# Kernel optimization log

Hardware: AMD Instinct MI355X
Metric: run time of the kernel (lower is better)

Reference implementation:

```python
import jax, jax.numpy as jnp
import numpy as np

B, L, F = 512, 128, 300          # batch, cycles per sample, curve length
D_MODEL = 512
D_LLM = 4096
E = 8                            # num_experts
G = 2                            # num_general_experts
TOP_K = 2
P = TOP_K / E                    # top-p threshold = topK / num_experts
EPS = 1e-9


def setup_inputs() -> dict:
    key = jax.random.key(0)
    ks = jax.random.split(key, 8)
    s_in = 1.0 / np.sqrt(3 * F).astype(np.float32)   # torch Linear init bound
    s_g = 1.0 / np.sqrt(D_LLM).astype(np.float32)
    return {
        "cycle_curve_data": jax.random.normal(ks[0], (B, L, 3, F), jnp.float32),
        "DKP_embeddings": jax.random.normal(ks[1], (B, D_LLM), jnp.float32),
        "W_exp": jax.random.uniform(ks[2], (E, 3 * F, D_MODEL), jnp.float32, -s_in, s_in),
        "b_exp": jax.random.uniform(ks[3], (E, D_MODEL), jnp.float32, -s_in, s_in),
        "W_gen": jax.random.uniform(ks[4], (G, 3 * F, D_MODEL), jnp.float32, -s_in, s_in),
        "b_gen": jax.random.uniform(ks[5], (G, D_MODEL), jnp.float32, -s_in, s_in),
        "W_gate": jax.random.uniform(ks[6], (D_LLM, E), jnp.float32, -s_g, s_g),
        "b_gate": jax.random.uniform(ks[7], (E,), jnp.float32, -s_g, s_g),
    }


def top_p_mask(logits, p):
    # softmax -> sort desc -> cumsum < p (first always kept) -> scatter back
    probs = jax.nn.softmax(logits, axis=-1)
    order = jnp.argsort(-probs, axis=-1)
    cum = jnp.cumsum(jnp.take_along_axis(probs, order, axis=-1), axis=-1)
    m = (cum < p).at[:, 0].set(True)
    rows = jnp.arange(logits.shape[0])[:, None]
    return jnp.zeros(logits.shape, bool).at[rows, order].set(m)


def reference(cycle_curve_data, DKP_embeddings, W_exp, b_exp, W_gen, b_gen, W_gate, b_gate):
    Bsz, Ls = cycle_curve_data.shape[:2]
    x = cycle_curve_data.reshape(Bsz, Ls, -1)            # [B, L, 3F]  (Flatten(start_dim=2))

    # gate (eval path: no noisy gating)
    logits = DKP_embeddings @ W_gate + b_gate            # [B, E]
    mask = top_p_mask(logits, P)
    w = jax.nn.softmax(logits, axis=1) * mask            # masked gate probs
    w = w / (jnp.sum(w, axis=1, keepdims=True) + EPS)    # renormalize (zeros stay zero)

    # dense equivalent of per-expert gather -> Linear -> weighted scatter-combine:
    # tokens with w[b,e]==0 contribute nothing, matching the sparse dispatcher.
    expert_outs = jnp.einsum('blf,efd->ebld', x, W_exp) + b_exp[:, None, None, :]  # [E,B,L,D]
    combined = jnp.einsum('be,ebld->bld', w, expert_outs).astype(jnp.bfloat16)     # [B,L,D] bf16

    # general experts run over the full batch and accumulate (bf16 + f32 -> f32)
    gen = jnp.einsum('blf,gfd->bld', x, W_gen) + jnp.sum(b_gen, axis=0)            # [B,L,D]
    return combined + gen
```

## Files before the change

kernel.cpp:

```cpp
#include <hip/hip_runtime.h>
#include <stdint.h>

#define NB   512
#define NL   128
#define NK   900
#define NKP  928
#define NKT  29
#define ND   512
#define NDLLM 4096
#define NE   8
#define ASTR 40

typedef __bf16 bf16x8 __attribute__((ext_vector_type(8)));
typedef float  f32x4  __attribute__((ext_vector_type(4)));

__device__ __forceinline__ unsigned short f2bf(float f) {
  union { float f; uint32_t u; } v; v.f = f;
  uint32_t u = v.u;
  return (unsigned short)((u + 0x7fffu + ((u >> 16) & 1u)) >> 16);
}

__global__ __launch_bounds__(256) void gate_kernel(
    const float* __restrict__ dkp,
    const float* __restrict__ Wg,
    const float* __restrict__ bg,
    int* __restrict__ eidx)
{
  const int b = blockIdx.x;
  const int t = threadIdx.x;
  float acc[8];
#pragma unroll
  for (int e = 0; e < 8; ++e) acc[e] = 0.f;
  const float* drow = dkp + (size_t)b * NDLLM;
  for (int k = t; k < NDLLM; k += 256) {
    float d = drow[k];
    const float4* w4 = (const float4*)(Wg + (size_t)k * 8);
    float4 w0 = w4[0], w1 = w4[1];
    acc[0] += d * w0.x; acc[1] += d * w0.y; acc[2] += d * w0.z; acc[3] += d * w0.w;
    acc[4] += d * w1.x; acc[5] += d * w1.y; acc[6] += d * w1.z; acc[7] += d * w1.w;
  }
#pragma unroll
  for (int e = 0; e < 8; ++e)
    for (int off = 32; off >= 1; off >>= 1)
      acc[e] += __shfl_down(acc[e], off, 64);

  __shared__ float red[4][8];
  const int wave = t >> 6, lane = t & 63;
  if (lane == 0) {
#pragma unroll
    for (int e = 0; e < 8; ++e) red[wave][e] = acc[e];
  }
  __syncthreads();
  if (t == 0) {
    float best = -1e30f; int bi = 0;
#pragma unroll
    for (int e = 0; e < 8; ++e) {
      float v = red[0][e] + red[1][e] + red[2][e] + red[3][e] + bg[e];
      if (v > best) { best = v; bi = e; }
    }
    eidx[b] = bi;
  }
}

__global__ __launch_bounds__(256) void pack_kernel(
    const float* __restrict__ Wexp,
    const float* __restrict__ Wgen,
    unsigned short* __restrict__ Wt)
{
  const int nt = blockIdx.x;
  const int kt = blockIdx.y;
  const int e  = blockIdx.z;
  const int k0 = kt * 32, n0 = nt * 64;
  __shared__ float tile[32][65];
  const int t = threadIdx.x;
#pragma unroll
  for (int i = 0; i < 8; ++i) {
    int idx = t + i * 256;
    int k = idx >> 6, n = idx & 63;
    int kg = k0 + k;
    float v = 0.f;
    if (kg < NK) {
      size_t off = (size_t)kg * ND + n0 + n;
      v = Wexp[(size_t)e * NK * ND + off] + Wgen[off] + Wgen[(size_t)NK * ND + off];
    }
    tile[k][n] = v;
  }
  __syncthreads();
#pragma unroll
  for (int i = 0; i < 8; ++i) {
    int idx = t + i * 256;
    int n = idx >> 5, k = idx & 31;
    Wt[((size_t)e * ND + n0 + n) * NKP + k0 + k] = f2bf(tile[k][n]);
  }
}

__global__ __launch_bounds__(256) void bias_kernel(
    const float* __restrict__ bexp, const float* __restrict__ bgen,
    float* __restrict__ btot)
{
  int i = blockIdx.x * 256 + threadIdx.x;
  int d = i & (ND - 1);
  btot[i] = bexp[i] + bgen[d] + bgen[ND + d];
}

__global__ __launch_bounds__(512, 2) void gemm_kernel(
    const float* __restrict__ x,
    const unsigned short* __restrict__ Wt,
    const float* __restrict__ btot,
    const int* __restrict__ eidx,
    float* __restrict__ out)
{
  __shared__ unsigned short As[2][NL * ASTR];
  __shared__ unsigned short Bs[2][ND * ASTR];

  const int b    = blockIdx.x;
  const int t    = threadIdx.x;
  const int lane = t & 63;
  const int w    = t >> 6;
  const int wm   = (w >> 2) * 64;
  const int wn   = (w & 3) * 128;
  const int ln   = lane & 15;
  const int kq   = lane >> 4;

  const int e = eidx[b];
  const float* xb = x + (size_t)b * NL * NK;
  const unsigned short* wtb = Wt + (size_t)e * ND * NKP;

  const int arow  = t >> 3;
  const int acol  = t & 7;
  const int brow  = t >> 2;
  const int bslot = t & 3;

  f32x4 acc[4][8];
  const f32x4 zero = {0.f, 0.f, 0.f, 0.f};
#pragma unroll
  for (int mi = 0; mi < 4; ++mi)
#pragma unroll
    for (int ni = 0; ni < 8; ++ni) acc[mi][ni] = zero;

  f32x4 aIn[2];
  uint4 bIn[4];

#define ISSUE_LOADS(K0)                                                       \
  {                                                                           \
    const int kg_ = (K0) + acol * 4;                                          \
    if (kg_ < NK) {                                                           \
      aIn[0] = *(const f32x4*)(xb + (size_t)arow * NK + kg_);                 \
      aIn[1] = *(const f32x4*)(xb + (size_t)(arow + 64) * NK + kg_);          \
    } else {                                                                  \
      aIn[0] = zero; aIn[1] = zero;                                           \
    }                                                                         \
    const unsigned short* bsrc_ = wtb + (K0) + bslot * 8;                     \
    _Pragma("unroll")                                                         \
    for (int p = 0; p < 4; ++p)                                               \
      bIn[p] = *(const uint4*)(bsrc_ + (size_t)(brow + p * 128) * NKP);       \
  }

#define WRITE_STAGE(BUF)                                                      \
  {                                                                           \
    _Pragma("unroll")                                                         \
    for (int p = 0; p < 2; ++p) {                                             \
      ushort4 h_;                                                             \
      h_.x = f2bf(aIn[p][0]); h_.y = f2bf(aIn[p][1]);                         \
      h_.z = f2bf(aIn[p][2]); h_.w = f2bf(aIn[p][3]);                         \
      *(ushort4*)&As[BUF][(arow + p * 64) * ASTR + acol * 4] = h_;            \
    }                                                                         \
    _Pragma("unroll")                                                         \
    for (int p = 0; p < 4; ++p)                                               \
      *(uint4*)&Bs[BUF][(brow + p * 128) * ASTR + bslot * 8] = bIn[p];        \
  }

#define COMPUTE(BUF)                                                          \
  {                                                                           \
    bf16x8 af_[4];                                                            \
    _Pragma("unroll")                                                         \
    for (int mi = 0; mi < 4; ++mi)                                            \
      af_[mi] = *(bf16x8*)&As[BUF][(wm + mi * 16 + ln) * ASTR + kq * 8];      \
    _Pragma("unroll")                                                         \
    for (int ni = 0; ni < 8; ++ni) {                                          \
      bf16x8 bv_ = *(bf16x8*)&Bs[BUF][(wn + ni * 16 + ln) * ASTR + kq * 8];   \
      _Pragma("unroll")                                                       \
      for (int mi = 0; mi < 4; ++mi)                                          \
        acc[mi][ni] = __builtin_amdgcn_mfma_f32_16x16x32_bf16(                \
            af_[mi], bv_, acc[mi][ni], 0, 0, 0);                              \
    }                                                                         \
  }

  ISSUE_LOADS(0);
  WRITE_STAGE(0);
  __syncthreads();

  int cur = 0;
  for (int kt = 0; kt < NKT - 1; ++kt) {
    ISSUE_LOADS((kt + 1) * 32);
    COMPUTE(cur);
    __syncthreads();
    WRITE_STAGE(cur ^ 1);
    __syncthreads();
    cur ^= 1;
  }
  COMPUTE(cur);

  const float* bt = btot + (size_t)e * ND;
#pragma unroll
  for (int ni = 0; ni < 8; ++ni) {
    const int ncol = wn + ni * 16 + ln;
    const float bias = bt[ncol];
#pragma unroll
    for (int mi = 0; mi < 4; ++mi) {
      const int l0 = wm + mi * 16 + kq * 4;
      float* op = out + ((size_t)b * NL + l0) * ND + ncol;
#pragma unroll
      for (int r = 0; r < 4; ++r)
        __builtin_nontemporal_store(acc[mi][ni][r] + bias, op + (size_t)r * ND);
    }
  }

#undef ISSUE_LOADS
#undef WRITE_STAGE
#undef COMPUTE
}

extern "C" void kernel_launch(void* const* d_in, const int* in_sizes, int n_in,
                              void* d_out, int out_size, void* d_ws, size_t ws_size,
                              hipStream_t stream) {
  const float* x     = (const float*)d_in[0];
  const float* dkp   = (const float*)d_in[1];
  const float* Wexp  = (const float*)d_in[2];
  const float* bexp  = (const float*)d_in[3];
  const float* Wgen  = (const float*)d_in[4];
  const float* bgen  = (const float*)d_in[5];
  const float* Wgate = (const float*)d_in[6];
  const float* bgate = (const float*)d_in[7];
  float* out = (float*)d_out;

  int*   eidx = (int*)d_ws;
  float* btot = (float*)((char*)d_ws + 2048);
  unsigned short* Wt = (unsigned short*)((char*)d_ws + 18432);

  gate_kernel<<<NB, 256, 0, stream>>>(dkp, Wgate, bgate, eidx);
  pack_kernel<<<dim3(8, NKT, NE), 256, 0, stream>>>(Wexp, Wgen, Wt);
  bias_kernel<<<16, 256, 0, stream>>>(bexp, bgen, btot);
  gemm_kernel<<<dim3(NB), 512, 0, stream>>>(x, Wt, btot, eidx, out);
}
```

Before: 502.9 us.

## Split GEMM output columns into two halves per batch to raise occupancy

Each batch's 128x512 output tile is now computed by two blocks, each covering 256 columns, so the grid doubles to 1024 blocks. Blocks are ordered so that both halves of a batch run close together and can share the x rows through cache. Smaller accumulators and LDS buffers let the launch bound request four blocks per CU instead of two. The catch is that each x slice is read and converted to bf16 twice, and nontemporal stores are swapped for plain stores.

```diff
diff --git a/kernel.cpp b/kernel.cpp
--- a/kernel.cpp
+++ b/kernel.cpp
@@ -7,6 +7,7 @@
 #define NKP  928
 #define NKT  29
 #define ND   512
+#define BN   256
 #define NDLLM 4096
 #define NE   8
 #define ASTR 40
@@ -103,7 +104,7 @@
   btot[i] = bexp[i] + bgen[d] + bgen[ND + d];
 }
 
-__global__ __launch_bounds__(512, 2) void gemm_kernel(
+__global__ __launch_bounds__(512, 4) void gemm_kernel(
     const float* __restrict__ x,
     const unsigned short* __restrict__ Wt,
     const float* __restrict__ btot,
@@ -111,49 +112,50 @@
     float* __restrict__ out)
 {
   __shared__ unsigned short As[2][NL * ASTR];
-  __shared__ unsigned short Bs[2][ND * ASTR];
-
-  const int b    = blockIdx.x;
+  __shared__ unsigned short Bs[2][BN * ASTR];
+
+  const int r   = blockIdx.x;
+  const int s   = r >> 3;
+  const int b   = (r & 7) + 8 * (s >> 1);
+  const int h   = s & 1;
+
   const int t    = threadIdx.x;
   const int lane = t & 63;
   const int w    = t >> 6;
   const int wm   = (w >> 2) * 64;
-  const int wn   = (w & 3) * 128;
+  const int wn   = (w & 3) * 64;
   const int ln   = lane & 15;
   const int kq   = lane >> 4;
 
   const int e = eidx[b];
   const float* xb = x + (size_t)b * NL * NK;
-  const unsigned short* wtb = Wt + (size_t)e * ND * NKP;
-
-  const int arow  = t >> 3;
-  const int acol  = t & 7;
-  const int brow  = t >> 2;
-  const int bslot = t & 3;
-
-  f32x4 acc[4][8];
+  const unsigned short* wtb = Wt + ((size_t)e * ND + (size_t)h * BN) * NKP;
+
+  const int ar0 = t >> 3, ac0 = t & 7;
+  const int br0 = t >> 2, bs0 = t & 3;
+
+  f32x4 acc[4][4];
   const f32x4 zero = {0.f, 0.f, 0.f, 0.f};
 #pragma unroll
   for (int mi = 0; mi < 4; ++mi)
 #pragma unroll
-    for (int ni = 0; ni < 8; ++ni) acc[mi][ni] = zero;
+    for (int ni = 0; ni < 4; ++ni) acc[mi][ni] = zero;
 
   f32x4 aIn[2];
-  uint4 bIn[4];
+  uint4 bIn[2];
 
 #define ISSUE_LOADS(K0)                                                       \
   {                                                                           \
-    const int kg_ = (K0) + acol * 4;                                          \
+    const int kg_ = (K0) + ac0 * 4;                                           \
     if (kg_ < NK) {                                                           \
-      aIn[0] = *(const f32x4*)(xb + (size_t)arow * NK + kg_);                 \
-      aIn[1] = *(const f32x4*)(xb + (size_t)(arow + 64) * NK + kg_);          \
+      aIn[0] = *(const f32x4*)(xb + (size_t)ar0 * NK + kg_);                  \
+      aIn[1] = *(const f32x4*)(xb + (size_t)(ar0 + 64) * NK + kg_);           \
     } else {                                                                  \
       aIn[0] = zero; aIn[1] = zero;                                           \
     }                                                                         \
-    const unsigned short* bsrc_ = wtb + (K0) + bslot * 8;                     \
-    _Pragma("unroll")                                                         \
-    for (int p = 0; p < 4; ++p)                                               \
-      bIn[p] = *(const uint4*)(bsrc_ + (size_t)(brow + p * 128) * NKP);       \
+    const unsigned short* bsrc_ = wtb + (K0) + bs0 * 8;                       \
+    bIn[0] = *(const uint4*)(bsrc_ + (size_t)br0 * NKP);                      \
+    bIn[1] = *(const uint4*)(bsrc_ + (size_t)(br0 + 128) * NKP);              \
   }
 
 #define WRITE_STAGE(BUF)                                                      \
@@ -163,26 +165,25 @@
       ushort4 h_;                                                             \
       h_.x = f2bf(aIn[p][0]); h_.y = f2bf(aIn[p][1]);                         \
       h_.z = f2bf(aIn[p][2]); h_.w = f2bf(aIn[p][3]);                         \
-      *(ushort4*)&As[BUF][(arow + p * 64) * ASTR + acol * 4] = h_;            \
+      *(ushort4*)&As[BUF][(ar0 + p * 64) * ASTR + ac0 * 4] = h_;              \
     }                                                                         \
-    _Pragma("unroll")                                                         \
-    for (int p = 0; p < 4; ++p)                                               \
-      *(uint4*)&Bs[BUF][(brow + p * 128) * ASTR + bslot * 8] = bIn[p];        \
+    *(uint4*)&Bs[BUF][(size_t)br0 * ASTR + bs0 * 8] = bIn[0];                 \
+    *(uint4*)&Bs[BUF][(size_t)(br0 + 128) * ASTR + bs0 * 8] = bIn[1];         \
   }
 
 #define COMPUTE(BUF)                                                          \
   {                                                                           \
-    bf16x8 af_[4];                                                            \
+    bf16x8 bv_[4];                                                            \
     _Pragma("unroll")                                                         \
-    for (int mi = 0; mi < 4; ++mi)                                            \
-      af_[mi] = *(bf16x8*)&As[BUF][(wm + mi * 16 + ln) * ASTR + kq * 8];      \
+    for (int ni = 0; ni < 4; ++ni)                                            \
+      bv_[ni] = *(bf16x8*)&Bs[BUF][(wn + ni * 16 + ln) * ASTR + kq * 8];      \
     _Pragma("unroll")                                                         \
-    for (int ni = 0; ni < 8; ++ni) {                                          \
-      bf16x8 bv_ = *(bf16x8*)&Bs[BUF][(wn + ni * 16 + ln) * ASTR + kq * 8];   \
+    for (int mi = 0; mi < 4; ++mi) {                                          \
+      bf16x8 af_ = *(bf16x8*)&As[BUF][(wm + mi * 16 + ln) * ASTR + kq * 8];   \
       _Pragma("unroll")                                                       \
-      for (int mi = 0; mi < 4; ++mi)                                          \
+      for (int ni = 0; ni < 4; ++ni)                                          \
         acc[mi][ni] = __builtin_amdgcn_mfma_f32_16x16x32_bf16(                \
-            af_[mi], bv_, acc[mi][ni], 0, 0, 0);                              \
+            af_, bv_[ni], acc[mi][ni], 0, 0, 0);                              \
     }                                                                         \
   }
 
@@ -203,16 +204,16 @@
 
   const float* bt = btot + (size_t)e * ND;
 #pragma unroll
-  for (int ni = 0; ni < 8; ++ni) {
-    const int ncol = wn + ni * 16 + ln;
+  for (int ni = 0; ni < 4; ++ni) {
+    const int ncol = h * BN + wn + ni * 16 + ln;
     const float bias = bt[ncol];
 #pragma unroll
     for (int mi = 0; mi < 4; ++mi) {
       const int l0 = wm + mi * 16 + kq * 4;
       float* op = out + ((size_t)b * NL + l0) * ND + ncol;
 #pragma unroll
-      for (int r = 0; r < 4; ++r)
-        __builtin_nontemporal_store(acc[mi][ni][r] + bias, op + (size_t)r * ND);
+      for (int rr = 0; rr < 4; ++rr)
+        op[(size_t)rr * ND] = acc[mi][ni][rr] + bias;
     }
   }
 
@@ -241,5 +242,5 @@
   gate_kernel<<<NB, 256, 0, stream>>>(dkp, Wgate, bgate, eidx);
   pack_kernel<<<dim3(8, NKT, NE), 256, 0, stream>>>(Wexp, Wgen, Wt);
   bias_kernel<<<16, 256, 0, stream>>>(bexp, bgen, btot);
-  gemm_kernel<<<dim3(NB), 512, 0, stream>>>(x, Wt, btot, eidx, out);
-}
+  gemm_kernel<<<dim3(NB * 2), 512, 0, stream>>>(x, Wt, btot, eidx, out);
+}
```

After: 482.7 us. 4.0% less time.
